# Optimization experiments

Measured on AMD Instinct MI355X. Metric: run time of the kernel, lower is better.

The kernel has to match this reference:

```python
import jax, jax.numpy as jnp
import numpy as np

N = 131072
HIDDEN = 1024
MIN_STD = 1e-5
PRIOR_SIGMA1 = 4.0 / np.sqrt(1.0)
PRIOR_SIGMA2 = 2.25 / np.sqrt(float(HIDDEN))


def setup_inputs() -> dict:
    key = jax.random.key(0)
    ks = jax.random.split(key, 13)
    f = lambda k, shape: jax.random.normal(k, shape, dtype=jnp.float32)
    return {
        "x": f(ks[0], (N, 1)),
        "W1_mu": f(ks[1], (HIDDEN, 1)),
        "W1_rho": f(ks[2], (HIDDEN, 1)),
        "b1_mu": f(ks[3], (HIDDEN,)),
        "b1_rho": f(ks[4], (HIDDEN,)),
        "W2_mu": f(ks[5], (2, HIDDEN)),
        "W2_rho": f(ks[6], (2, HIDDEN)),
        "b2_mu": f(ks[7], (2,)),
        "b2_rho": f(ks[8], (2,)),
        "eps_W1": f(ks[9], (HIDDEN, 1)),
        "eps_b1": f(ks[10], (HIDDEN,)),
        "eps_W2": f(ks[11], (2, HIDDEN)),
        "eps_b2": f(ks[12], (2,)),
    }


def _kl(mu, sigma, prior_sigma):
    # KL( N(mu, sigma) || N(0, prior_sigma) ), summed over elements
    return 0.5 * jnp.sum(
        2.0 * jnp.log(prior_sigma / sigma) - 1.0
        + (sigma / prior_sigma) ** 2
        + (mu / prior_sigma) ** 2
    )


def _bbb_linear(x, W_mu, W_rho, b_mu, b_rho, eps_W, eps_b, prior_sigma):
    W_sigma = jax.nn.softplus(W_rho)
    b_sigma = jax.nn.softplus(b_rho)
    W = W_mu + W_sigma * eps_W  # [out, in]
    b = b_mu + b_sigma * eps_b  # [out]
    out = x @ W.T + b  # [N, out]
    kl = _kl(W_mu, W_sigma, prior_sigma) + _kl(b_mu, b_sigma, prior_sigma)
    return out, kl


def reference(x, W1_mu, W1_rho, b1_mu, b1_rho, W2_mu, W2_rho, b2_mu, b2_rho,
              eps_W1, eps_b1, eps_W2, eps_b2):
    h1, kl1 = _bbb_linear(x, W1_mu, W1_rho, b1_mu, b1_rho, eps_W1, eps_b1, PRIOR_SIGMA1)
    h3, kl3 = _bbb_linear(jax.nn.relu(h1), W2_mu, W2_rho, b2_mu, b2_rho, eps_W2, eps_b2, PRIOR_SIGMA2)
    means = h3[:, 0]
    stds = MIN_STD + jax.nn.softplus(h3[:, 1])
    kl = kl1 + kl3
    return means, stds, kl
```

## Files before the change

kernel.cpp:

```cpp
#include <hip/hip_runtime.h>
#include <math.h>

#define N_SAMPLES 131072
#define HIDDEN 1024
#define SEGS 8
#define SEG_UNITS (HIDDEN / SEGS)
#define PAIRS 128
#define SAMPLES_PER_BLOCK (2 * PAIRS)

typedef float v2f __attribute__((ext_vector_type(2)));

__device__ __forceinline__ float softplusf(float v) {
    return fmaxf(v, 0.0f) + log1pf(expf(-fabsf(v)));
}
__device__ __forceinline__ float kl_term_f(float mu, float sigma, float inv_prior) {
    float r = sigma * inv_prior;
    float m = mu * inv_prior;
    return 0.5f * (-2.0f * logf(r) - 1.0f + r * r + m * m);
}

__global__ __launch_bounds__(1024) void bbb_prep(
    const float* __restrict__ W1_mu, const float* __restrict__ W1_rho,
    const float* __restrict__ b1_mu, const float* __restrict__ b1_rho,
    const float* __restrict__ W2_mu, const float* __restrict__ W2_rho,
    const float* __restrict__ b2_mu, const float* __restrict__ b2_rho,
    const float* __restrict__ eps_W1, const float* __restrict__ eps_b1,
    const float* __restrict__ eps_W2, const float* __restrict__ eps_b2,
    float4* __restrict__ params,
    float* __restrict__ kl_out)
{
    __shared__ double s_part[16];
    const int tid = threadIdx.x;

    const float ip1 = 0.25f;
    const float ip2 = 32.0f / 2.25f;

    float w1mu  = W1_mu[tid],          w1rho  = W1_rho[tid];
    float b1mu  = b1_mu[tid],          b1rho  = b1_rho[tid];
    float w2amu = W2_mu[tid],          w2arho = W2_rho[tid];
    float w2bmu = W2_mu[HIDDEN + tid], w2brho = W2_rho[HIDDEN + tid];

    float sg_w1  = softplusf(w1rho);
    float sg_b1  = softplusf(b1rho);
    float sg_w2a = softplusf(w2arho);
    float sg_w2b = softplusf(w2brho);

    float w1  = fmaf(sg_w1,  eps_W1[tid],          w1mu);
    float bb1 = fmaf(sg_b1,  eps_b1[tid],          b1mu);
    float w2a = fmaf(sg_w2a, eps_W2[tid],          w2amu);
    float w2b = fmaf(sg_w2b, eps_W2[HIDDEN + tid], w2bmu);

    params[tid] = make_float4(w1, bb1, w2a, w2b);

    double kl = (double)kl_term_f(w1mu,  sg_w1,  ip1)
              + (double)kl_term_f(b1mu,  sg_b1,  ip1)
              + (double)kl_term_f(w2amu, sg_w2a, ip2)
              + (double)kl_term_f(w2bmu, sg_w2b, ip2);

    if (tid < 2) {
        kl += (double)kl_term_f(b2_mu[tid], softplusf(b2_rho[tid]), ip2);
    }
    if (tid == 0) {
        float bb2a = fmaf(softplusf(b2_rho[0]), eps_b2[0], b2_mu[0]);
        float bb2b = fmaf(softplusf(b2_rho[1]), eps_b2[1], b2_mu[1]);
        params[HIDDEN] = make_float4(bb2a, bb2b, 0.0f, 0.0f);
    }

    #pragma unroll
    for (int off = 32; off > 0; off >>= 1) kl += __shfl_down(kl, off, 64);
    if ((tid & 63) == 0) s_part[tid >> 6] = kl;
    __syncthreads();
    if (tid == 0) {
        double t = 0.0;
        #pragma unroll
        for (int i = 0; i < 16; ++i) t += s_part[i];
        *kl_out = (float)t;
    }
}

__global__ __launch_bounds__(1024) void bbb_eval(
    const float* __restrict__ x,
    const float4* __restrict__ params,
    float* __restrict__ means,
    float* __restrict__ stds)
{
    __shared__ float4 s_part[SEGS][PAIRS];

    const int tid  = threadIdx.x;
    const int pair = tid & (PAIRS - 1);
    const int seg  = __builtin_amdgcn_readfirstlane(tid >> 7);
    const int base = blockIdx.x * SAMPLES_PER_BLOCK;

    const v2f xv = *(const v2f*)(x + base + 2 * pair);

    const float4* __restrict__ p = params + seg * SEG_UNITS;

    v2f aa = {0.0f, 0.0f};
    v2f ab = {0.0f, 0.0f};
    #pragma unroll 8
    for (int j = 0; j < SEG_UNITS; ++j) {
        float4 q = p[j];
        v2f h = __builtin_elementwise_fma((v2f)q.x, xv, (v2f)q.y);
        h = __builtin_elementwise_max(h, (v2f)0.0f);
        aa = __builtin_elementwise_fma(h, (v2f)q.z, aa);
        ab = __builtin_elementwise_fma(h, (v2f)q.w, ab);
    }
    s_part[seg][pair] = make_float4(aa.x, aa.y, ab.x, ab.y);
    __syncthreads();

    if (tid < PAIRS) {
        const float4 b2 = params[HIDDEN];
        float4 acc = s_part[0][tid];
        #pragma unroll
        for (int s = 1; s < SEGS; ++s) {
            float4 v = s_part[s][tid];
            acc.x += v.x; acc.y += v.y; acc.z += v.z; acc.w += v.w;
        }
        float m0 = acc.x + b2.x;
        float m1 = acc.y + b2.x;
        float u0 = acc.z + b2.y;
        float u1 = acc.w + b2.y;
        *(float2*)(means + base + 2 * tid) = make_float2(m0, m1);
        *(float2*)(stds  + base + 2 * tid) =
            make_float2(1e-5f + softplusf(u0), 1e-5f + softplusf(u1));
    }
}

extern "C" void kernel_launch(void* const* d_in, const int* in_sizes, int n_in,
                              void* d_out, int out_size, void* d_ws, size_t ws_size,
                              hipStream_t stream) {
    const float* x      = (const float*)d_in[0];
    const float* W1_mu  = (const float*)d_in[1];
    const float* W1_rho = (const float*)d_in[2];
    const float* b1_mu  = (const float*)d_in[3];
    const float* b1_rho = (const float*)d_in[4];
    const float* W2_mu  = (const float*)d_in[5];
    const float* W2_rho = (const float*)d_in[6];
    const float* b2_mu  = (const float*)d_in[7];
    const float* b2_rho = (const float*)d_in[8];
    const float* eps_W1 = (const float*)d_in[9];
    const float* eps_b1 = (const float*)d_in[10];
    const float* eps_W2 = (const float*)d_in[11];
    const float* eps_b2 = (const float*)d_in[12];

    float* out = (float*)d_out;
    float4* params_ws = (float4*)d_ws;

    bbb_prep<<<1, HIDDEN, 0, stream>>>(
        W1_mu, W1_rho, b1_mu, b1_rho, W2_mu, W2_rho, b2_mu, b2_rho,
        eps_W1, eps_b1, eps_W2, eps_b2,
        params_ws, out + 2 * N_SAMPLES);

    bbb_eval<<<N_SAMPLES / SAMPLES_PER_BLOCK, 1024, 0, stream>>>(
        x, params_ws, out, out + N_SAMPLES);
}
```

Before: 95.15 us.

## Fuse parameter prep into eval kernel, recompute sampled weights per block into LDS

Merges the single-block parameter sampling kernel and the evaluation kernel into one launch. Each of the 512 blocks recomputes the 1024 sampled weights with softplus and stores them in shared memory, and only block 0 computes and reduces the KL term. This removes a kernel launch, the serial dependency on one tiny block, and the global round trip of params. In exchange every block does redundant transcendental work and reads parameters from LDS instead of through scalar/global cached loads, which may be slower in the inner loop.

```diff
diff --git a/kernel.cpp b/kernel.cpp
--- a/kernel.cpp
+++ b/kernel.cpp
@@ -19,17 +19,23 @@
     return 0.5f * (-2.0f * logf(r) - 1.0f + r * r + m * m);
 }
 
-__global__ __launch_bounds__(1024) void bbb_prep(
+__global__ __launch_bounds__(1024) void bbb_fused(
+    const float* __restrict__ x,
     const float* __restrict__ W1_mu, const float* __restrict__ W1_rho,
     const float* __restrict__ b1_mu, const float* __restrict__ b1_rho,
     const float* __restrict__ W2_mu, const float* __restrict__ W2_rho,
     const float* __restrict__ b2_mu, const float* __restrict__ b2_rho,
     const float* __restrict__ eps_W1, const float* __restrict__ eps_b1,
     const float* __restrict__ eps_W2, const float* __restrict__ eps_b2,
-    float4* __restrict__ params,
+    float* __restrict__ means,
+    float* __restrict__ stds,
     float* __restrict__ kl_out)
 {
-    __shared__ double s_part[16];
+    __shared__ float4 s_params[HIDDEN];
+    __shared__ float2 s_b2;
+    __shared__ float4 s_part[SEGS][PAIRS];
+    __shared__ double s_red[16];
+
     const int tid = threadIdx.x;
 
     const float ip1 = 0.25f;
@@ -45,55 +51,42 @@
     float sg_w2a = softplusf(w2arho);
     float sg_w2b = softplusf(w2brho);
 
-    float w1  = fmaf(sg_w1,  eps_W1[tid],          w1mu);
-    float bb1 = fmaf(sg_b1,  eps_b1[tid],          b1mu);
-    float w2a = fmaf(sg_w2a, eps_W2[tid],          w2amu);
-    float w2b = fmaf(sg_w2b, eps_W2[HIDDEN + tid], w2bmu);
-
-    params[tid] = make_float4(w1, bb1, w2a, w2b);
-
-    double kl = (double)kl_term_f(w1mu,  sg_w1,  ip1)
-              + (double)kl_term_f(b1mu,  sg_b1,  ip1)
-              + (double)kl_term_f(w2amu, sg_w2a, ip2)
-              + (double)kl_term_f(w2bmu, sg_w2b, ip2);
-
-    if (tid < 2) {
-        kl += (double)kl_term_f(b2_mu[tid], softplusf(b2_rho[tid]), ip2);
-    }
+    s_params[tid] = make_float4(fmaf(sg_w1,  eps_W1[tid],          w1mu),
+                                fmaf(sg_b1,  eps_b1[tid],          b1mu),
+                                fmaf(sg_w2a, eps_W2[tid],          w2amu),
+                                fmaf(sg_w2b, eps_W2[HIDDEN + tid], w2bmu));
     if (tid == 0) {
-        float bb2a = fmaf(softplusf(b2_rho[0]), eps_b2[0], b2_mu[0]);
-        float bb2b = fmaf(softplusf(b2_rho[1]), eps_b2[1], b2_mu[1]);
-        params[HIDDEN] = make_float4(bb2a, bb2b, 0.0f, 0.0f);
+        s_b2 = make_float2(fmaf(softplusf(b2_rho[0]), eps_b2[0], b2_mu[0]),
+                           fmaf(softplusf(b2_rho[1]), eps_b2[1], b2_mu[1]));
     }
 
-    #pragma unroll
-    for (int off = 32; off > 0; off >>= 1) kl += __shfl_down(kl, off, 64);
-    if ((tid & 63) == 0) s_part[tid >> 6] = kl;
+    if (blockIdx.x == 0) {
+        double kl = (double)kl_term_f(w1mu,  sg_w1,  ip1)
+                  + (double)kl_term_f(b1mu,  sg_b1,  ip1)
+                  + (double)kl_term_f(w2amu, sg_w2a, ip2)
+                  + (double)kl_term_f(w2bmu, sg_w2b, ip2);
+        if (tid < 2) {
+            kl += (double)kl_term_f(b2_mu[tid], softplusf(b2_rho[tid]), ip2);
+        }
+        #pragma unroll
+        for (int off = 32; off > 0; off >>= 1) kl += __shfl_down(kl, off, 64);
+        if ((tid & 63) == 0) s_red[tid >> 6] = kl;
+        __syncthreads();
+        if (tid == 0) {
+            double t = 0.0;
+            #pragma unroll
+            for (int i = 0; i < 16; ++i) t += s_red[i];
+            *kl_out = (float)t;
+        }
+    }
     __syncthreads();
-    if (tid == 0) {
-        double t = 0.0;
-        #pragma unroll
-        for (int i = 0; i < 16; ++i) t += s_part[i];
-        *kl_out = (float)t;
-    }
-}
 
-__global__ __launch_bounds__(1024) void bbb_eval(
-    const float* __restrict__ x,
-    const float4* __restrict__ params,
-    float* __restrict__ means,
-    float* __restrict__ stds)
-{
-    __shared__ float4 s_part[SEGS][PAIRS];
-
-    const int tid  = threadIdx.x;
     const int pair = tid & (PAIRS - 1);
     const int seg  = __builtin_amdgcn_readfirstlane(tid >> 7);
     const int base = blockIdx.x * SAMPLES_PER_BLOCK;
 
     const v2f xv = *(const v2f*)(x + base + 2 * pair);
-
-    const float4* __restrict__ p = params + seg * SEG_UNITS;
+    const float4* p = &s_params[seg * SEG_UNITS];
 
     v2f aa = {0.0f, 0.0f};
     v2f ab = {0.0f, 0.0f};
@@ -109,7 +102,7 @@
     __syncthreads();
 
     if (tid < PAIRS) {
-        const float4 b2 = params[HIDDEN];
+        const float2 b2 = s_b2;
         float4 acc = s_part[0][tid];
         #pragma unroll
         for (int s = 1; s < SEGS; ++s) {
@@ -144,13 +137,10 @@
     const float* eps_b2 = (const float*)d_in[12];
 
     float* out = (float*)d_out;
-    float4* params_ws = (float4*)d_ws;
 
-    bbb_prep<<<1, HIDDEN, 0, stream>>>(
+    bbb_fused<<<N_SAMPLES / SAMPLES_PER_BLOCK, 1024, 0, stream>>>(
+        x,
         W1_mu, W1_rho, b1_mu, b1_rho, W2_mu, W2_rho, b2_mu, b2_rho,
         eps_W1, eps_b1, eps_W2, eps_b2,
-        params_ws, out + 2 * N_SAMPLES);
-
-    bbb_eval<<<N_SAMPLES / SAMPLES_PER_BLOCK, 1024, 0, stream>>>(
-        x, params_ws, out, out + N_SAMPLES);
+        out, out + N_SAMPLES, out + 2 * N_SAMPLES);
 }
```

Result: slower. 98.43 us (+3.5%).
